# Kernel tuning notes

Measured on AMD Instinct MI355X. Metric: run time of the kernel, lower is better.

## Reference

```python
import jax, jax.numpy as jnp
import numpy as np

B, T, C = 2, 4096, 512
H = 8
D = C // H  # head_dim = 64


def setup_inputs() -> dict:
    key = jax.random.key(0)
    ks = jax.random.split(key, 9)
    s = 0.02
    return {
        "x": jax.random.normal(ks[0], (B, T, C), dtype=jnp.float32),
        "wq": jax.random.normal(ks[1], (C, C), dtype=jnp.float32) * s,
        "bq": jnp.zeros((C,), dtype=jnp.float32),
        "wk": jax.random.normal(ks[2], (C, C), dtype=jnp.float32) * s,
        "bk": jnp.zeros((C,), dtype=jnp.float32),
        "wv": jax.random.normal(ks[3], (C, C), dtype=jnp.float32) * s,
        "bv": jnp.zeros((C,), dtype=jnp.float32),
        "wo": jax.random.normal(ks[4], (C, C), dtype=jnp.float32) * s,
        "bo": jnp.zeros((C,), dtype=jnp.float32),
    }


def reference(x, wq, bq, wk, bk, wv, bv, wo, bo):
    Bx, Tx, Cx = x.shape
    # projections: y = x @ W^T + b (torch Linear convention: W is [out, in])
    q = (x @ wq.T + bq).reshape(Bx, Tx, H, D).transpose(0, 2, 1, 3)  # [B,H,T,D]
    k = (x @ wk.T + bk).reshape(Bx, Tx, H, D).transpose(0, 2, 1, 3)
    v = (x @ wv.T + bv).reshape(Bx, Tx, H, D).transpose(0, 2, 1, 3)
    scores = jnp.einsum("bhqd,bhkd->bhqk", q, k) * (D ** -0.5)  # [B,H,T,T]
    causal = jnp.tril(jnp.ones((Tx, Tx), dtype=bool))
    scores = jnp.where(causal, scores, -jnp.inf)
    weights = jax.nn.softmax(scores, axis=-1)
    o = jnp.einsum("bhqk,bhkd->bhqd", weights, v)  # [B,H,T,D]
    o = o.transpose(0, 2, 1, 3).reshape(Bx, Tx, Cx)
    return o @ wo.T + bo
```

## Files before the change

kernel.cpp:

```cpp
#include <hip/hip_runtime.h>
#include <math.h>

static constexpr int Bb = 2;
static constexpr int Tt = 4096;
static constexpr int Cc = 512;
static constexpr int Hh = 8;
static constexpr int Dd = 64;
static constexpr int Mtot = Bb * Tt;

#define QSCALE 0.1803368801111f
#define NTICK 1024

typedef __attribute__((ext_vector_type(8)))  short   short8;
typedef __attribute__((ext_vector_type(4)))  float   f32x4;
typedef __attribute__((ext_vector_type(16))) float   f32x16;
typedef __attribute__((ext_vector_type(4)))  unsigned int   uint4v;
typedef __attribute__((ext_vector_type(4)))  unsigned short ushort4v;

__device__ inline unsigned short f2bf(float f) {
    unsigned int u = __float_as_uint(f);
    u += 0x7fffu + ((u >> 16) & 1u);
    return (unsigned short)(u >> 16);
}
__device__ inline float bf2f(unsigned short u) {
    return __uint_as_float((unsigned int)u << 16);
}

__device__ inline unsigned int cvtpk_bf16(float a, float b) {
    unsigned int r;
    asm("v_cvt_pk_bf16_f32 %0, %1, %2" : "=v"(r) : "v"(a), "v"(b));
    return r;
}

__device__ inline int SW(int row) { return (row ^ (row >> 3)) & 7; }

__device__ inline void gload16(const void* g, void* lds) {
    __builtin_amdgcn_global_load_lds(
        (const __attribute__((address_space(1))) void*)g,
        (__attribute__((address_space(3))) void*)lds, 16, 0, 0);
}

__global__ __launch_bounds__(256)
void cast_all(const float* __restrict__ x,
              const float* __restrict__ w0, const float* __restrict__ w1,
              const float* __restrict__ w2, const float* __restrict__ w3,
              unsigned short* __restrict__ xb, unsigned short* __restrict__ wb,
              int* __restrict__ ctr) {
    const int bid = (int)blockIdx.x;
    if (bid == 0 && threadIdx.x == 0) *ctr = 0;
    const float* src;
    unsigned short* dst;
    size_t i;
    if (bid < 2048) {
        src = x; dst = xb;
        i = ((size_t)bid * 256 + threadIdx.x) * 8;
    } else {
        const float* srcs[4] = {w0, w1, w2, w3};
        const int wi = (bid - 2048) >> 7;
        src = srcs[wi];
        dst = wb + (size_t)wi * (Cc * Cc);
        i = ((size_t)((bid - 2048) & 127) * 256 + threadIdx.x) * 8;
    }
    const float4 a = *reinterpret_cast<const float4*>(src + i);
    const float4 b = *reinterpret_cast<const float4*>(src + i + 4);
    short8 o;
    o[0] = (short)f2bf(a.x); o[1] = (short)f2bf(a.y);
    o[2] = (short)f2bf(a.z); o[3] = (short)f2bf(a.w);
    o[4] = (short)f2bf(b.x); o[5] = (short)f2bf(b.y);
    o[6] = (short)f2bf(b.z); o[7] = (short)f2bf(b.w);
    *reinterpret_cast<short8*>(dst + i) = o;
}

__global__ __launch_bounds__(256)
void proj_qkv(const unsigned short* __restrict__ A, const unsigned short* __restrict__ Wall,
              const float* __restrict__ bq, const float* __restrict__ bk,
              const float* __restrict__ bv,
              unsigned short* __restrict__ qo, unsigned short* __restrict__ ko,
              unsigned short* __restrict__ vo) {
    __shared__ unsigned short As[128][72];
    __shared__ unsigned short Bs[128][72];

    const int which = blockIdx.z;
    const unsigned short* Wb = Wall + (size_t)which * Cc * Cc;
    const float* bias = (which == 0) ? bq : (which == 1) ? bk : bv;
    unsigned short* outp = (which == 0) ? qo : (which == 1) ? ko : vo;
    const float scale = (which == 0) ? QSCALE : 1.0f;

    const int tid = threadIdx.x;
    const int lane = tid & 63;
    const int w = tid >> 6;
    const int wr = w >> 1, wc = w & 1;
    const int l15 = lane & 15, lg = lane >> 4;
    const int m0 = blockIdx.x * 128, n0 = blockIdx.y * 128;

    f32x4 acc[4][4] = {};

    for (int k0 = 0; k0 < Cc; k0 += 64) {
        #pragma unroll
        for (int i = 0; i < 4; ++i) {
            const int idx = tid + i * 256;
            const int row = idx >> 3, g = idx & 7;
            *reinterpret_cast<short8*>(&As[row][g * 8]) =
                *reinterpret_cast<const short8*>(&A[(size_t)(m0 + row) * Cc + k0 + g * 8]);
            *reinterpret_cast<short8*>(&Bs[row][g * 8]) =
                *reinterpret_cast<const short8*>(&Wb[(size_t)(n0 + row) * Cc + k0 + g * 8]);
        }
        __syncthreads();
        #pragma unroll
        for (int kh = 0; kh < 2; ++kh) {
            short8 a[4], b[4];
            #pragma unroll
            for (int mi = 0; mi < 4; ++mi)
                a[mi] = *reinterpret_cast<const short8*>(
                    &As[wr * 64 + mi * 16 + l15][kh * 32 + lg * 8]);
            #pragma unroll
            for (int nj = 0; nj < 4; ++nj)
                b[nj] = *reinterpret_cast<const short8*>(
                    &Bs[wc * 64 + nj * 16 + l15][kh * 32 + lg * 8]);
            #pragma unroll
            for (int mi = 0; mi < 4; ++mi)
                #pragma unroll
                for (int nj = 0; nj < 4; ++nj)
                    acc[mi][nj] = __builtin_amdgcn_mfma_f32_16x16x32_bf16(a[mi], b[nj], acc[mi][nj], 0, 0, 0);
        }
        __syncthreads();
    }

    #pragma unroll
    for (int mi = 0; mi < 4; ++mi) {
        #pragma unroll
        for (int nj = 0; nj < 4; ++nj) {
            const int col = n0 + wc * 64 + nj * 16 + l15;
            const float bvv = bias[col];
            if (which == 2) {
                const int mbase = m0 + wr * 64 + mi * 16 + lg * 4;
                const int b_ = mbase >> 12, t = mbase & (Tt - 1);
                const int h = col >> 6, d = col & 63;
                ushort4v o;
                #pragma unroll
                for (int r = 0; r < 4; ++r)
                    o[r] = f2bf(acc[mi][nj][r] + bvv);
                *reinterpret_cast<ushort4v*>(
                    &outp[(((size_t)b_ * Hh + h) * Dd + d) * Tt + t]) = o;
            } else {
                #pragma unroll
                for (int r = 0; r < 4; ++r) {
                    const int row = m0 + wr * 64 + mi * 16 + lg * 4 + r;
                    const int b_ = row >> 12, t = row & (Tt - 1);
                    const int h = col >> 6, d = col & 63;
                    outp[(((size_t)b_ * Hh + h) * Tt + t) * Dd + d] =
                        f2bf((acc[mi][nj][r] + bvv) * scale);
                }
            }
        }
    }
}

__global__ __launch_bounds__(256)
void proj_out(const unsigned short* __restrict__ opart, const float* __restrict__ lp,
              const unsigned short* __restrict__ Wb,
              const float* __restrict__ bias, float* __restrict__ outp) {
    __shared__ unsigned short As[64][32];
    __shared__ unsigned short Bs[128][32];

    const int tid = threadIdx.x;
    const int lane = tid & 63;
    const int w = tid >> 6;
    const int l15 = lane & 15, lg = lane >> 4;
    const int m0 = blockIdx.x * 64, n0 = blockIdx.y * 128;

    const int row_a = tid >> 2;
    const int sg = tid & 3;
    const int m = m0 + row_a;
    const int b_a = m >> 12, t_a = m & (Tt - 1);
    const size_t cs = (size_t)16 * Tt;

    const int srow = (w << 4) + (lane >> 2);
    const int sgb = lane & 3;

    f32x4 acc[4][2] = {};

    for (int k0 = 0; k0 < Cc; k0 += 32) {
        {
            const int c0 = k0 + sg * 8;
            const int h = c0 >> 6, d0 = c0 & 63;
            const size_t rbase = ((size_t)b_a * Hh + h) * Tt + t_a;
            const float lsum = lp[rbase] + lp[cs + rbase] +
                               lp[2 * cs + rbase] + lp[3 * cs + rbase];
            const float inv = 1.f / lsum;
            float s[8] = {};
            #pragma unroll
            for (int chk = 0; chk < 4; ++chk) {
                const short8 v8 = *reinterpret_cast<const short8*>(
                    &opart[(chk * cs + rbase) * 64 + d0]);
                #pragma unroll
                for (int e = 0; e < 8; ++e) s[e] += bf2f((unsigned short)v8[e]);
            }
            short8 o8;
            #pragma unroll
            for (int e = 0; e < 8; ++e) o8[e] = (short)f2bf(s[e] * inv);
            *reinterpret_cast<short8*>(&As[row_a][((sg ^ (row_a & 3))) * 8]) = o8;
        }
        #pragma unroll
        for (int i = 0; i < 2; ++i) {
            const int row = 64 * i + srow;
            const int gc = (sgb ^ (row & 3)) * 8;
            gload16(&Wb[(size_t)(n0 + row) * Cc + k0 + gc], &Bs[64 * i + (w << 4)][0]);
        }
        __syncthreads();

        short8 a[4], b[2];
        const int rg = (lg ^ (l15 & 3)) * 8;
        #pragma unroll
        for (int mi = 0; mi < 4; ++mi)
            a[mi] = *reinterpret_cast<const short8*>(&As[mi * 16 + l15][rg]);
        #pragma unroll
        for (int nj = 0; nj < 2; ++nj)
            b[nj] = *reinterpret_cast<const short8*>(&Bs[w * 32 + nj * 16 + l15][rg]);
        #pragma unroll
        for (int mi = 0; mi < 4; ++mi)
            #pragma unroll
            for (int nj = 0; nj < 2; ++nj)
                acc[mi][nj] = __builtin_amdgcn_mfma_f32_16x16x32_bf16(a[mi], b[nj], acc[mi][nj], 0, 0, 0);
        __syncthreads();
    }

    #pragma unroll
    for (int mi = 0; mi < 4; ++mi) {
        #pragma unroll
        for (int nj = 0; nj < 2; ++nj) {
            const int col = n0 + w * 32 + nj * 16 + l15;
            const float bv = bias[col];
            #pragma unroll
            for (int r = 0; r < 4; ++r) {
                const int row = m0 + mi * 16 + lg * 4 + r;
                outp[(size_t)row * Cc + col] = acc[mi][nj][r] + bv;
            }
        }
    }
}

__global__ __launch_bounds__(512)
void attn_mfma(const unsigned short* __restrict__ qb, const unsigned short* __restrict__ kb,
               const unsigned short* __restrict__ vtb,
               unsigned short* __restrict__ opart, float* __restrict__ lp,
               int* __restrict__ ctr) {
    __shared__ unsigned short Ks[3][64][64];
    __shared__ unsigned short Vts[3][64][64];
    __shared__ int tkt;

    const int tid = threadIdx.x;
    const int w = tid >> 6;
    const int lane = tid & 63;
    const int l31 = lane & 31, hi = lane >> 5;

    const int r0 = (w << 3) + (lane >> 3);
    const int gk0 = ((lane & 7) ^ SW(r0)) * 8;

    for (;;) {
        __syncthreads();
        if (tid == 0) tkt = atomicAdd(ctr, 1);
        __syncthreads();
        const int t = tkt;
        if (t >= NTICK) break;

        const int qt = 15 - (t >> 6);
        const int ch = (t >> 4) & 3;
        const int bh = t & 15;
        const int t0 = (qt + 1) * ch;
        const int t1 = (qt + 1) * (ch + 1);

        const int qg = qt * 256 + w * 32 + l31;

        short8 qf[4];
        {
            const unsigned short* qp = qb + ((size_t)bh * Tt + qg) * Dd + hi * 8;
            #pragma unroll
            for (int sl = 0; sl < 4; ++sl)
                qf[sl] = *reinterpret_cast<const short8*>(qp + sl * 16);
        }

        const unsigned short* kb_h = kb + (size_t)bh * Tt * Dd;
        const unsigned short* vt_h = vtb + (size_t)bh * Dd * Tt;

        auto STAGE = [&](int kt_, int slot) {
            const int n64 = kt_ * 64;
            gload16(kb_h + (size_t)(n64 + r0) * Dd + gk0, &Ks[slot][(w << 3)][0]);
            gload16(vt_h + (size_t)r0 * Tt + n64 + gk0, &Vts[slot][(w << 3)][0]);
        };

        f32x16 oaccA[2] = {};
        f32x16 oaccB[2] = {};
        float lrow = 0.f;

        const int qmax_w = qt * 256 + w * 32 + 31;
        const int qmin_w = qt * 256 + w * 32;

        STAGE(t0, 0);
        if (t0 + 1 < t1) STAGE(t0 + 1, 1);

        int cur = 0;
        for (int kt = t0; kt < t1; ++kt) {
            if (kt + 1 < t1) {
                asm volatile("s_waitcnt vmcnt(2)" ::: "memory");
            } else {
                asm volatile("s_waitcnt vmcnt(0)" ::: "memory");
            }
            __builtin_amdgcn_s_barrier();
            __builtin_amdgcn_sched_barrier(0);

            if (kt + 2 < t1) {
                const int stg = (cur + 2 >= 3) ? (cur - 1) : (cur + 2);
                STAGE(kt + 2, stg);
            }

            if (kt * 64 <= qmax_w) {
                f32x16 sacc[2];
                __builtin_amdgcn_s_setprio(1);
                #pragma unroll
                for (int f = 0; f < 2; ++f) {
                    f32x16 z = {};
                    const int krow = f * 32 + l31;
                    const int sw = SW(krow);
                    #pragma unroll
                    for (int sl = 0; sl < 4; ++sl) {
                        const short8 kf = *reinterpret_cast<const short8*>(
                            &Ks[cur][krow][((2 * sl + hi) ^ sw) * 8]);
                        z = __builtin_amdgcn_mfma_f32_32x32x16_bf16(kf, qf[sl], z, 0, 0, 0);
                    }
                    sacc[f] = z;
                }
                __builtin_amdgcn_s_setprio(0);

                if (kt * 64 + 63 > qmin_w) {
                    #pragma unroll
                    for (int f = 0; f < 2; ++f)
                        #pragma unroll
                        for (int r = 0; r < 16; ++r) {
                            const int kvg = kt * 64 + f * 32 + (r & 3) + 8 * (r >> 2) + 4 * hi;
                            if (kvg > qg) sacc[f][r] = -INFINITY;
                        }
                }

                #pragma unroll
                for (int f = 0; f < 2; ++f) {
                    #pragma unroll
                    for (int r = 0; r < 16; ++r)
                        sacc[f][r] = exp2f(sacc[f][r]);

                    float t8[8];
                    #pragma unroll
                    for (int r = 0; r < 8; ++r) t8[r] = sacc[f][r] + sacc[f][r + 8];
                    #pragma unroll
                    for (int r = 0; r < 4; ++r) t8[r] += t8[r + 4];
                    t8[0] += t8[2];
                    t8[1] += t8[3];
                    lrow += t8[0] + t8[1];

                    f32x16* oacc = (f == 0) ? oaccA : oaccB;
                    #pragma unroll
                    for (int s2 = 0; s2 < 2; ++s2) {
                        const int b0 = s2 * 8;
                        unsigned int c01 = cvtpk_bf16(sacc[f][b0 + 0], sacc[f][b0 + 1]);
                        unsigned int c23 = cvtpk_bf16(sacc[f][b0 + 2], sacc[f][b0 + 3]);
                        unsigned int c45 = cvtpk_bf16(sacc[f][b0 + 4], sacc[f][b0 + 5]);
                        unsigned int c67 = cvtpk_bf16(sacc[f][b0 + 6], sacc[f][b0 + 7]);
                        asm("v_permlane32_swap_b32 %0, %1" : "+v"(c01), "+v"(c45));
                        asm("v_permlane32_swap_b32 %0, %1" : "+v"(c23), "+v"(c67));
                        uint4v paw;
                        paw[0] = c01; paw[1] = c23; paw[2] = c45; paw[3] = c67;
                        const short8 pa = *reinterpret_cast<short8*>(&paw);
                        const int g = 4 * f + 2 * s2;
                        __builtin_amdgcn_s_setprio(1);
                        #pragma unroll
                        for (int nb = 0; nb < 2; ++nb) {
                            const int vrow = nb * 32 + l31;
                            const short8 vf = *reinterpret_cast<const short8*>(
                                &Vts[cur][vrow][((g + hi) ^ SW(vrow)) * 8]);
                            oacc[nb] = __builtin_amdgcn_mfma_f32_32x32x16_bf16(pa, vf, oacc[nb], 0, 0, 0);
                        }
                        __builtin_amdgcn_s_setprio(0);
                    }
                }
            }

            cur = (cur == 2) ? 0 : cur + 1;
        }

        const float lf = lrow + __shfl_xor(lrow, 32);
        const size_t pbase = ((size_t)ch * 16 + bh) * Tt;
        if (hi == 0) lp[pbase + qg] = lf;
        #pragma unroll
        for (int r = 0; r < 16; ++r) {
            const int qr = (r & 3) + 8 * (r >> 2) + 4 * hi;
            const int tg = qt * 256 + w * 32 + qr;
            unsigned short* dst = opart + (pbase + tg) * 64 + l31;
            dst[0]  = f2bf(oaccA[0][r] + oaccB[0][r]);
            dst[32] = f2bf(oaccA[1][r] + oaccB[1][r]);
        }
    }
}

extern "C" void kernel_launch(void* const* d_in, const int* in_sizes, int n_in,
                              void* d_out, int out_size, void* d_ws, size_t ws_size,
                              hipStream_t stream) {
    const float* x  = (const float*)d_in[0];
    const float* wq = (const float*)d_in[1];
    const float* bq = (const float*)d_in[2];
    const float* wk = (const float*)d_in[3];
    const float* bk = (const float*)d_in[4];
    const float* wv = (const float*)d_in[5];
    const float* bv = (const float*)d_in[6];
    const float* wo = (const float*)d_in[7];
    const float* bo = (const float*)d_in[8];
    float* out = (float*)d_out;

    const size_t nTok = (size_t)Mtot * Cc;
    const size_t nW   = (size_t)Cc * Cc;

    unsigned short* xb    = (unsigned short*)d_ws;
    unsigned short* wqb   = xb + nTok;
    unsigned short* wob   = wqb + 3 * nW;
    unsigned short* qbuf  = wqb + 4 * nW;
    unsigned short* kbuf  = qbuf + nTok;
    unsigned short* vtbuf = kbuf + nTok;
    unsigned short* opart = vtbuf + nTok;
    float* lp  = (float*)(opart + (size_t)4 * 16 * Tt * 64);
    int*   ctr = (int*)(lp + (size_t)4 * 16 * Tt);

    cast_all<<<dim3(2560), 256, 0, stream>>>(x, wq, wk, wv, wo, xb, wqb, ctr);

    proj_qkv<<<dim3(Mtot / 128, Cc / 128, 3), 256, 0, stream>>>(
        xb, wqb, bq, bk, bv, qbuf, kbuf, vtbuf);

    attn_mfma<<<dim3(512), 512, 0, stream>>>(qbuf, kbuf, vtbuf, opart, lp, ctr);

    proj_out<<<dim3(Mtot / 64, Cc / 128), 256, 0, stream>>>(opart, lp, wob, bo, out);
}
```

Baseline: 138.9 us.

## Fuse fp32-to-bf16 casts into projection GEMM tile loads and drop cast kernel

Removes the separate cast_all kernel and converts x and the weights from fp32 to bf16 on the fly while loading GEMM tiles into LDS, using packed bf16 convert instructions. The attention counter reset moves into proj_qkv. This saves a kernel launch and the write and re-read of bf16 copies of the inputs. In exchange the projections read fp32 data, twice the bytes, and reconvert it in every tile that reuses it. proj_out also loses its async global-to-LDS loads for the weights.

```diff
diff --git a/kernel.cpp b/kernel.cpp
--- a/kernel.cpp
+++ b/kernel.cpp
@@ -32,6 +32,17 @@
     return r;
 }
 
+__device__ inline short8 cvt8(const float* p) {
+    const float4 a = *reinterpret_cast<const float4*>(p);
+    const float4 b = *reinterpret_cast<const float4*>(p + 4);
+    uint4v u;
+    u[0] = cvtpk_bf16(a.x, a.y);
+    u[1] = cvtpk_bf16(a.z, a.w);
+    u[2] = cvtpk_bf16(b.x, b.y);
+    u[3] = cvtpk_bf16(b.z, b.w);
+    return *reinterpret_cast<short8*>(&u);
+}
+
 __device__ inline int SW(int row) { return (row ^ (row >> 3)) & 7; }
 
 __device__ inline void gload16(const void* g, void* lds) {
@@ -41,50 +52,24 @@
 }
 
 __global__ __launch_bounds__(256)
-void cast_all(const float* __restrict__ x,
-              const float* __restrict__ w0, const float* __restrict__ w1,
-              const float* __restrict__ w2, const float* __restrict__ w3,
-              unsigned short* __restrict__ xb, unsigned short* __restrict__ wb,
-              int* __restrict__ ctr) {
-    const int bid = (int)blockIdx.x;
-    if (bid == 0 && threadIdx.x == 0) *ctr = 0;
-    const float* src;
-    unsigned short* dst;
-    size_t i;
-    if (bid < 2048) {
-        src = x; dst = xb;
-        i = ((size_t)bid * 256 + threadIdx.x) * 8;
-    } else {
-        const float* srcs[4] = {w0, w1, w2, w3};
-        const int wi = (bid - 2048) >> 7;
-        src = srcs[wi];
-        dst = wb + (size_t)wi * (Cc * Cc);
-        i = ((size_t)((bid - 2048) & 127) * 256 + threadIdx.x) * 8;
-    }
-    const float4 a = *reinterpret_cast<const float4*>(src + i);
-    const float4 b = *reinterpret_cast<const float4*>(src + i + 4);
-    short8 o;
-    o[0] = (short)f2bf(a.x); o[1] = (short)f2bf(a.y);
-    o[2] = (short)f2bf(a.z); o[3] = (short)f2bf(a.w);
-    o[4] = (short)f2bf(b.x); o[5] = (short)f2bf(b.y);
-    o[6] = (short)f2bf(b.z); o[7] = (short)f2bf(b.w);
-    *reinterpret_cast<short8*>(dst + i) = o;
-}
-
-__global__ __launch_bounds__(256)
-void proj_qkv(const unsigned short* __restrict__ A, const unsigned short* __restrict__ Wall,
+void proj_qkv(const float* __restrict__ x,
+              const float* __restrict__ wq, const float* __restrict__ wk,
+              const float* __restrict__ wv,
               const float* __restrict__ bq, const float* __restrict__ bk,
               const float* __restrict__ bv,
               unsigned short* __restrict__ qo, unsigned short* __restrict__ ko,
-              unsigned short* __restrict__ vo) {
+              unsigned short* __restrict__ vo, int* __restrict__ ctr) {
     __shared__ unsigned short As[128][72];
     __shared__ unsigned short Bs[128][72];
 
     const int which = blockIdx.z;
-    const unsigned short* Wb = Wall + (size_t)which * Cc * Cc;
+    const float* Wsel = (which == 0) ? wq : (which == 1) ? wk : wv;
     const float* bias = (which == 0) ? bq : (which == 1) ? bk : bv;
     unsigned short* outp = (which == 0) ? qo : (which == 1) ? ko : vo;
     const float scale = (which == 0) ? QSCALE : 1.0f;
+
+    if (blockIdx.x == 0 && blockIdx.y == 0 && blockIdx.z == 0 && threadIdx.x == 0)
+        *ctr = 0;
 
     const int tid = threadIdx.x;
     const int lane = tid & 63;
@@ -101,9 +86,9 @@
             const int idx = tid + i * 256;
             const int row = idx >> 3, g = idx & 7;
             *reinterpret_cast<short8*>(&As[row][g * 8]) =
-                *reinterpret_cast<const short8*>(&A[(size_t)(m0 + row) * Cc + k0 + g * 8]);
+                cvt8(&x[(size_t)(m0 + row) * Cc + k0 + g * 8]);
             *reinterpret_cast<short8*>(&Bs[row][g * 8]) =
-                *reinterpret_cast<const short8*>(&Wb[(size_t)(n0 + row) * Cc + k0 + g * 8]);
+                cvt8(&Wsel[(size_t)(n0 + row) * Cc + k0 + g * 8]);
         }
         __syncthreads();
         #pragma unroll
@@ -158,7 +143,7 @@
 
 __global__ __launch_bounds__(256)
 void proj_out(const unsigned short* __restrict__ opart, const float* __restrict__ lp,
-              const unsigned short* __restrict__ Wb,
+              const float* __restrict__ wo,
               const float* __restrict__ bias, float* __restrict__ outp) {
     __shared__ unsigned short As[64][32];
     __shared__ unsigned short Bs[128][32];
@@ -174,9 +159,6 @@
     const int m = m0 + row_a;
     const int b_a = m >> 12, t_a = m & (Tt - 1);
     const size_t cs = (size_t)16 * Tt;
-
-    const int srow = (w << 4) + (lane >> 2);
-    const int sgb = lane & 3;
 
     f32x4 acc[4][2] = {};
 
@@ -203,9 +185,10 @@
         }
         #pragma unroll
         for (int i = 0; i < 2; ++i) {
-            const int row = 64 * i + srow;
-            const int gc = (sgb ^ (row & 3)) * 8;
-            gload16(&Wb[(size_t)(n0 + row) * Cc + k0 + gc], &Bs[64 * i + (w << 4)][0]);
+            const int idx = tid + i * 256;
+            const int row = idx >> 2, g = idx & 3;
+            const short8 o8 = cvt8(&wo[(size_t)(n0 + row) * Cc + k0 + g * 8]);
+            *reinterpret_cast<short8*>(&Bs[row][((g ^ (row & 3))) * 8]) = o8;
         }
         __syncthreads();
 
@@ -416,24 +399,18 @@
     float* out = (float*)d_out;
 
     const size_t nTok = (size_t)Mtot * Cc;
-    const size_t nW   = (size_t)Cc * Cc;
-
-    unsigned short* xb    = (unsigned short*)d_ws;
-    unsigned short* wqb   = xb + nTok;
-    unsigned short* wob   = wqb + 3 * nW;
-    unsigned short* qbuf  = wqb + 4 * nW;
+
+    unsigned short* qbuf  = (unsigned short*)d_ws;
     unsigned short* kbuf  = qbuf + nTok;
     unsigned short* vtbuf = kbuf + nTok;
     unsigned short* opart = vtbuf + nTok;
     float* lp  = (float*)(opart + (size_t)4 * 16 * Tt * 64);
     int*   ctr = (int*)(lp + (size_t)4 * 16 * Tt);
 
-    cast_all<<<dim3(2560), 256, 0, stream>>>(x, wq, wk, wv, wo, xb, wqb, ctr);
-
     proj_qkv<<<dim3(Mtot / 128, Cc / 128, 3), 256, 0, stream>>>(
-        xb, wqb, bq, bk, bv, qbuf, kbuf, vtbuf);
+        x, wq, wk, wv, bq, bk, bv, qbuf, kbuf, vtbuf, ctr);
 
     attn_mfma<<<dim3(512), 512, 0, stream>>>(qbuf, kbuf, vtbuf, opart, lp, ctr);
 
-    proj_out<<<dim3(Mtot / 64, Cc / 128), 256, 0, stream>>>(opart, lp, wob, bo, out);
-}
+    proj_out<<<dim3(Mtot / 64, Cc / 128), 256, 0, stream>>>(opart, lp, wo, bo, out);
+}
```

Result: slower. 142.7 us (+2.7%).
